# Kernel tuning notes

Hardware: AMD Instinct MI355X
Metric: run time of the kernel (lower is better)

## Reference

```python
import jax, jax.numpy as jnp
import numpy as np

N, E, H, D = 4096, 512, 8, 64
SCALE = np.sqrt(D).astype(np.float32)

def setup_inputs() -> dict:
    key = jax.random.key(0)
    ks = jax.random.split(key, 9)
    s = 1.0 / np.sqrt(E)
    return {
        'x':  jax.random.normal(ks[0], (N, E), dtype=jnp.float32),
        'Wq': jax.random.normal(ks[1], (E, E), dtype=jnp.float32) * s,
        'bq': jax.random.normal(ks[2], (E,), dtype=jnp.float32) * s,
        'Wk': jax.random.normal(ks[3], (E, E), dtype=jnp.float32) * s,
        'bk': jax.random.normal(ks[4], (E,), dtype=jnp.float32) * s,
        'Wv': jax.random.normal(ks[5], (E, E), dtype=jnp.float32) * s,
        'bv': jax.random.normal(ks[6], (E,), dtype=jnp.float32) * s,
        'Wo': jax.random.normal(ks[7], (E, E), dtype=jnp.float32) * s,
        'bo': jax.random.normal(ks[8], (E,), dtype=jnp.float32) * s,
    }

def reference(x, Wq, bq, Wk, bk, Wv, bv, Wo, bo):
    n = x.shape[0]
    # Linear layers (torch Linear: y = x @ W.T + b)
    Q = (x @ Wq.T + bq).reshape(n, H, D)  # [N,H,D]
    K = (x @ Wk.T + bk).reshape(n, H, D)
    V = (x @ Wv.T + bv).reshape(n, H, D)
    # scores over the batch axis: [H,N,N]
    scores = jnp.einsum('nhd,mhd->hnm', Q, K) / SCALE
    attn = jax.nn.softmax(scores, axis=-1)  # [H,N,N]
    ctx = jnp.einsum('hnm,mhd->nhd', attn, V).reshape(n, E)
    out = ctx @ Wo.T + bo  # [N,E]
    return out, attn, Q, K, V
```

## Files before the change

kernel.cpp:

```cpp
#include <hip/hip_runtime.h>
#include <hip/hip_bf16.h>
#include <math.h>

#define TOK   4096
#define EDIM  512
#define HEADS 8
#define DHEAD 64

typedef __attribute__((ext_vector_type(8))) short short8v;
typedef __attribute__((ext_vector_type(4))) float float4v;
typedef __attribute__((ext_vector_type(4))) unsigned int uint4v;

#define SC2 0.180336880111f

__device__ __forceinline__ unsigned short f2bf(float f) {
    unsigned int u = __float_as_uint(f);
    unsigned int r = (u + 0x7FFFu + ((u >> 16) & 1u)) >> 16;
    return (unsigned short)r;
}
__device__ __forceinline__ unsigned int packbf_tr(float lo, float hi) {
    return __builtin_amdgcn_perm(__float_as_uint(hi), __float_as_uint(lo), 0x07060302u);
}
__device__ __forceinline__ float fast_exp2(float x) {
#if __has_builtin(__builtin_amdgcn_exp2f)
    return __builtin_amdgcn_exp2f(x);
#else
    return __expf(x * 0.69314718f);
#endif
}

__global__ __launch_bounds__(256) void to_bf16_all(
    const float* __restrict__ x,
    const float* __restrict__ wq, const float* __restrict__ wk,
    const float* __restrict__ wv, const float* __restrict__ wo,
    unsigned short* __restrict__ xb,
    unsigned short* __restrict__ wqb, unsigned short* __restrict__ wkb,
    unsigned short* __restrict__ wvb, unsigned short* __restrict__ wob)
{
    const int bid = blockIdx.x;
    const float* src; unsigned short* dst; int idx;
    if (bid < 1024) { src = x; dst = xb; idx = bid; }
    else {
        const int k = (bid - 1024) >> 7;
        idx = (bid - 1024) & 127;
        src = (k == 0) ? wq : (k == 1) ? wk : (k == 2) ? wv : wo;
        dst = (k == 0) ? wqb : (k == 1) ? wkb : (k == 2) ? wvb : wob;
    }
    const int off = idx * 2048 + threadIdx.x * 8;
    float4 a = *(const float4*)(src + off);
    float4 b = *(const float4*)(src + off + 4);
    short8v o;
    o[0] = (short)f2bf(a.x); o[1] = (short)f2bf(a.y);
    o[2] = (short)f2bf(a.z); o[3] = (short)f2bf(a.w);
    o[4] = (short)f2bf(b.x); o[5] = (short)f2bf(b.y);
    o[6] = (short)f2bf(b.z); o[7] = (short)f2bf(b.w);
    *(short8v*)(dst + off) = o;
}

template<int MODE>
__global__ __launch_bounds__(256, 3) void gemm512(
    const unsigned short* __restrict__ A,
    const unsigned short* __restrict__ W,
    const float* __restrict__ bias,
    float* __restrict__ Y,
    unsigned short* __restrict__ sec)
{
    __shared__ alignas(16) char sA[2][8192];
    __shared__ alignas(16) char sB[2][8192];

    const int t = threadIdx.x;
    const int lane = t & 63, w = t >> 6;
    const int l15 = lane & 15, g4 = lane >> 4;
    const int wr = w >> 1, wc = w & 1;
    const int m0 = blockIdx.y * 64, n0 = blockIdx.x * 64;

    short8v areg[2], breg[2];

#define GL(kk) { _Pragma("unroll") for (int j = 0; j < 2; ++j) { \
        const int unit_ = j * 256 + t, row_ = unit_ >> 3, u_ = unit_ & 7; \
        areg[j] = *(const short8v*)(A + (size_t)(m0 + row_) * 512 + (kk) * 64 + u_ * 8); \
        breg[j] = *(const short8v*)(W + (size_t)(n0 + row_) * 512 + (kk) * 64 + u_ * 8); } }
#define GW(b) { _Pragma("unroll") for (int j = 0; j < 2; ++j) { \
        const int unit_ = j * 256 + t, row_ = unit_ >> 3, u_ = unit_ & 7; \
        const int byt_ = row_ * 128 + ((u_ ^ (row_ & 7)) * 16); \
        *(short8v*)(sA[b] + byt_) = areg[j]; *(short8v*)(sB[b] + byt_) = breg[j]; } }

    float4v acc[2][2];
#pragma unroll
    for (int mi = 0; mi < 2; ++mi)
#pragma unroll
        for (int ni = 0; ni < 2; ++ni) acc[mi][ni] = (float4v){0.f, 0.f, 0.f, 0.f};

    GL(0); GW(0); __syncthreads();

#pragma unroll 2
    for (int kk = 0; kk < 8; ++kk) {
        if (kk < 7) GL(kk + 1);
        const char* cA = sA[kk & 1];
        const char* cB = sB[kk & 1];
        short8v af[2][2], bf[2][2];
#pragma unroll
        for (int mi = 0; mi < 2; ++mi)
#pragma unroll
            for (int kh = 0; kh < 2; ++kh) {
                const int row = wr * 32 + mi * 16 + l15;
                af[mi][kh] = *(const short8v*)(cA + row * 128 + (((kh * 4 + g4) ^ (l15 & 7)) * 16));
            }
#pragma unroll
        for (int ni = 0; ni < 2; ++ni)
#pragma unroll
            for (int kh = 0; kh < 2; ++kh) {
                const int row = wc * 32 + ni * 16 + l15;
                bf[ni][kh] = *(const short8v*)(cB + row * 128 + (((kh * 4 + g4) ^ (l15 & 7)) * 16));
            }
        __builtin_amdgcn_s_setprio(1);
#pragma unroll
        for (int mi = 0; mi < 2; ++mi)
#pragma unroll
            for (int ni = 0; ni < 2; ++ni) {
                acc[mi][ni] = __builtin_amdgcn_mfma_f32_16x16x32_bf16(af[mi][0], bf[ni][0], acc[mi][ni], 0, 0, 0);
                acc[mi][ni] = __builtin_amdgcn_mfma_f32_16x16x32_bf16(af[mi][1], bf[ni][1], acc[mi][ni], 0, 0, 0);
            }
        __builtin_amdgcn_s_setprio(0);
        if (kk < 7) GW((kk + 1) & 1);
        __syncthreads();
    }

#pragma unroll
    for (int mi = 0; mi < 2; ++mi)
#pragma unroll
        for (int ni = 0; ni < 2; ++ni) {
            const int col = n0 + wc * 32 + ni * 16 + l15;
            const float bb = bias[col];
#pragma unroll
            for (int r = 0; r < 4; ++r) {
                const int row = m0 + wr * 32 + mi * 16 + g4 * 4 + r;
                const float v = acc[mi][ni][r] + bb;
                Y[(size_t)row * 512 + col] = v;
                if (MODE == 1)
                    sec[((size_t)(col >> 6) * TOK + row) * 64 + (col & 63)] = f2bf(v);
                if (MODE == 2)
                    sec[((size_t)(col >> 6) * 64 + (col & 63)) * TOK + row] = f2bf(v);
            }
        }
#undef GL
#undef GW
}

__global__ __launch_bounds__(256, 4) void fused_attn(
    const float* __restrict__ Q,
    const unsigned short* __restrict__ Kb,
    const unsigned short* __restrict__ Vt,
    float* __restrict__ attn,
    unsigned short* __restrict__ ctxb)
{
    __shared__ alignas(16) char lds_main[32768];
    __shared__ alignas(16) char ldsP[8192];

    const int t = threadIdx.x;
    const int lane = t & 63, w = t >> 6;
    const int l15 = lane & 15, g4 = lane >> 4;
    const int bid = blockIdx.x;
    const int h  = bid & 7;
    const int n0 = (bid >> 3) * 32;
    const int rg = w >> 1;
    const int mh = w & 1;
    const int xsw = (l15 & 7) << 1;

    const unsigned short* KbH = Kb + (size_t)h * TOK * DHEAD;
    const unsigned short* VtH = Vt + (size_t)h * DHEAD * TOK;
    char* myP = ldsP + w * 2048;
    float* redS = (float*)lds_main;

    short8v bq[2];
    {
        const float* qp = Q + (size_t)(n0 + rg * 16 + l15) * EDIM + h * DHEAD + g4 * 8;
#pragma unroll
        for (int ks = 0; ks < 2; ++ks) {
            float4 u = *(const float4*)(qp + ks * 32);
            float4 v = *(const float4*)(qp + ks * 32 + 4);
            bq[ks][0] = (short)f2bf(u.x); bq[ks][1] = (short)f2bf(u.y);
            bq[ks][2] = (short)f2bf(u.z); bq[ks][3] = (short)f2bf(u.w);
            bq[ks][4] = (short)f2bf(v.x); bq[ks][5] = (short)f2bf(v.y);
            bq[ks][6] = (short)f2bf(v.z); bq[ks][7] = (short)f2bf(v.w);
        }
    }

    short8v kreg[4], vreg[4];
#define LK(c) { _Pragma("unroll") for (int j = 0; j < 4; ++j) { \
        const int unit_ = j * 256 + t, row_ = unit_ >> 3, u_ = unit_ & 7; \
        kreg[j] = *(const short8v*)(KbH + (size_t)((c) * 128 + row_) * 64 + u_ * 8); } }
#define WK(base) { _Pragma("unroll") for (int j = 0; j < 4; ++j) { \
        const int unit_ = j * 256 + t, row_ = unit_ >> 3, u_ = unit_ & 7; \
        *(short8v*)((base) + row_ * 128 + ((u_ ^ (row_ & 7)) * 16)) = kreg[j]; } }
#define LV(c) { _Pragma("unroll") for (int j = 0; j < 4; ++j) { \
        const int unit_ = j * 256 + t, row_ = unit_ >> 4, u_ = unit_ & 15; \
        vreg[j] = *(const short8v*)(VtH + (size_t)row_ * TOK + (c) * 128 + u_ * 8); } }
#define WV(base) { _Pragma("unroll") for (int j = 0; j < 4; ++j) { \
        const int unit_ = j * 256 + t, row_ = unit_ >> 4, u_ = unit_ & 15; \
        *(short8v*)((base) + row_ * 256 + ((u_ ^ (row_ & 7)) * 16)) = vreg[j]; } }

    float psum = 0.f;
    LK(0); WK(lds_main); __syncthreads();
    for (int c = 0; c < 32; ++c) {
        if (c < 31) LK(c + 1);
        const char* sKc = lds_main + (c & 1) * 16384;
#pragma unroll
        for (int mt = 0; mt < 4; ++mt) {
            const int row = mh * 64 + mt * 16 + l15;
            short8v k0 = *(const short8v*)(sKc + row * 128 + ((g4 ^ (l15 & 7)) * 16));
            short8v k1 = *(const short8v*)(sKc + row * 128 + (((4 + g4) ^ (l15 & 7)) * 16));
            __builtin_amdgcn_s_setprio(1);
            float4v s = (float4v){0.f, 0.f, 0.f, 0.f};
            s = __builtin_amdgcn_mfma_f32_16x16x32_bf16(k0, bq[0], s, 0, 0, 0);
            s = __builtin_amdgcn_mfma_f32_16x16x32_bf16(k1, bq[1], s, 0, 0, 0);
            __builtin_amdgcn_s_setprio(0);
#pragma unroll
            for (int r = 0; r < 4; ++r)
                psum += fast_exp2(s[r] * SC2);
        }
        if (c < 31) WK(lds_main + ((c + 1) & 1) * 16384);
        __syncthreads();
    }
    psum += __shfl_xor(psum, 16, 64);
    psum += __shfl_xor(psum, 32, 64);
    if (lane < 16)
        redS[(rg * 16 + lane) * 2 + mh] = psum;
    __syncthreads();
    const float inv = 1.0f / (redS[(rg * 16 + l15) * 2] + redS[(rg * 16 + l15) * 2 + 1]);
    __syncthreads();

    float* aH = attn + ((size_t)h * TOK + n0 + rg * 16 + l15) * TOK;
    float4v cacc[4];
#pragma unroll
    for (int dt = 0; dt < 4; ++dt) cacc[dt] = (float4v){0.f, 0.f, 0.f, 0.f};

    char* sK2 = lds_main;
    char* sV2 = lds_main + 16384;

    LK(0); LV(0); WK(sK2); WV(sV2); __syncthreads();
    for (int c = 0; c < 32; ++c) {
        if (c < 31) { LK(c + 1); LV(c + 1); }
        const int mbase = c * 128 + mh * 64;
#pragma unroll
        for (int mt = 0; mt < 4; ++mt) {
            const int row = mh * 64 + mt * 16 + l15;
            short8v k0 = *(const short8v*)(sK2 + row * 128 + ((g4 ^ (l15 & 7)) * 16));
            short8v k1 = *(const short8v*)(sK2 + row * 128 + (((4 + g4) ^ (l15 & 7)) * 16));
            __builtin_amdgcn_s_setprio(1);
            float4v s = (float4v){0.f, 0.f, 0.f, 0.f};
            s = __builtin_amdgcn_mfma_f32_16x16x32_bf16(k0, bq[0], s, 0, 0, 0);
            s = __builtin_amdgcn_mfma_f32_16x16x32_bf16(k1, bq[1], s, 0, 0, 0);
            __builtin_amdgcn_s_setprio(0);
            float4v p;
#pragma unroll
            for (int r = 0; r < 4; ++r)
                p[r] = fast_exp2(s[r] * SC2) * inv;
            *(float4v*)(aH + mbase + mt * 16 + g4 * 4) = p;
            const unsigned int u0 = packbf_tr(p[0], p[1]);
            const unsigned int u1 = packbf_tr(p[2], p[3]);
            *(uint2*)(myP + l15 * 128 + (((mt * 4 + g4) ^ xsw) << 3)) =
                make_uint2(u0, u1);
        }
        __builtin_amdgcn_s_setprio(1);
#pragma unroll
        for (int ks2 = 0; ks2 < 2; ++ks2) {
            const uint4v pr = *(const uint4v*)(myP + l15 * 128 +
                                               (((ks2 * 8 + g4 * 2) ^ xsw) << 3));
            const short8v pa = __builtin_bit_cast(short8v, pr);
#pragma unroll
            for (int dt = 0; dt < 4; ++dt) {
                const int rowv = dt * 16 + l15;
                const int uu = (mh * 8 + ks2 * 4 + g4) ^ (l15 & 7);
                short8v vf = *(const short8v*)(sV2 + rowv * 256 + uu * 16);
                cacc[dt] = __builtin_amdgcn_mfma_f32_16x16x32_bf16(pa, vf, cacc[dt], 0, 0, 0);
            }
        }
        __builtin_amdgcn_s_setprio(0);
        __syncthreads();
        if (c < 31) { WK(sK2); WV(sV2); __syncthreads(); }
    }

    float* osh = (float*)lds_main + (size_t)w * 1088;
#pragma unroll
    for (int dt = 0; dt < 4; ++dt)
#pragma unroll
        for (int r = 0; r < 4; ++r)
            osh[(g4 * 4 + r) * 68 + dt * 16 + l15] = cacc[dt][r];
    __syncthreads();
    {
        const int n = t >> 3, dq = t & 7;
        const int w0 = (n >> 4) * 2;
        const float* o0 = (const float*)lds_main + (size_t)w0 * 1088 + (n & 15) * 68 + dq * 8;
        unsigned short ob[8];
#pragma unroll
        for (int q = 0; q < 2; ++q) {
            float4 s = *(const float4*)(o0 + q * 4);
            const float4 a = *(const float4*)(o0 + 1088 + q * 4);
            s.x += a.x; s.y += a.y; s.z += a.z; s.w += a.w;
            ob[q * 4 + 0] = f2bf(s.x); ob[q * 4 + 1] = f2bf(s.y);
            ob[q * 4 + 2] = f2bf(s.z); ob[q * 4 + 3] = f2bf(s.w);
        }
        *(short8v*)(ctxb + (size_t)(n0 + n) * EDIM + h * DHEAD + dq * 8) =
            *(const short8v*)&ob[0];
    }
#undef LK
#undef WK
#undef LV
#undef WV
}

extern "C" void kernel_launch(void* const* d_in, const int* in_sizes, int n_in,
                              void* d_out, int out_size, void* d_ws, size_t ws_size,
                              hipStream_t stream) {
    (void)in_sizes; (void)n_in; (void)out_size; (void)ws_size;

    const float* x  = (const float*)d_in[0];
    const float* Wq = (const float*)d_in[1];
    const float* bq = (const float*)d_in[2];
    const float* Wk = (const float*)d_in[3];
    const float* bk = (const float*)d_in[4];
    const float* Wv = (const float*)d_in[5];
    const float* bv = (const float*)d_in[6];
    const float* Wo = (const float*)d_in[7];
    const float* bo = (const float*)d_in[8];

    float* out  = (float*)d_out;
    float* attn = out  + (size_t)TOK * EDIM;
    float* Qf   = attn + (size_t)HEADS * TOK * TOK;
    float* Kf   = Qf   + (size_t)TOK * EDIM;
    float* Vf   = Kf   + (size_t)TOK * EDIM;

    char* wsb = (char*)d_ws;
    unsigned short* xb   = (unsigned short*)wsb;
    unsigned short* wqb  = (unsigned short*)(wsb + (4u << 20));
    unsigned short* wkb  = (unsigned short*)(wsb + (4u << 20) + (512u << 10));
    unsigned short* wvb  = (unsigned short*)(wsb + (5u << 20));
    unsigned short* wob  = (unsigned short*)(wsb + (5u << 20) + (512u << 10));
    unsigned short* KbW  = (unsigned short*)(wsb + (6u << 20));
    unsigned short* VtW  = (unsigned short*)(wsb + (10u << 20));
    unsigned short* ctxb = xb;

    to_bf16_all<<<1536, 256, 0, stream>>>(x, Wq, Wk, Wv, Wo, xb, wqb, wkb, wvb, wob);

    dim3 gg(EDIM / 64, TOK / 64);
    gemm512<0><<<gg, 256, 0, stream>>>(xb, wqb, bq, Qf, nullptr);
    gemm512<1><<<gg, 256, 0, stream>>>(xb, wkb, bk, Kf, KbW);
    gemm512<2><<<gg, 256, 0, stream>>>(xb, wvb, bv, Vf, VtW);

    fused_attn<<<1024, 256, 0, stream>>>(Qf, KbW, VtW, attn, ctxb);

    gemm512<0><<<gg, 256, 0, stream>>>(ctxb, wob, bo, out, nullptr);
}
```

Baseline: 206.4 us.

## Load K and V fragments directly from global into registers, drop LDS staging

The first pass, which only accumulates the softmax denominator, now loads K fragments straight from global memory into double-buffered registers, with no LDS writes and no per-chunk barriers. In the second pass, V fragments are loaded directly into registers in MFMA operand layout instead of being staged through LDS. K now uses a double-buffered LDS area with one barrier per chunk instead of two. This cuts LDS traffic and synchronisation, but raises register pressure, which may lower occupancy, and relies on uncoalesced per-lane global loads being served from cache.

```diff
diff --git a/kernel.cpp b/kernel.cpp
--- a/kernel.cpp
+++ b/kernel.cpp
@@ -186,25 +186,63 @@
         }
     }
 
-    short8v kreg[4], vreg[4];
+    float psum = 0.f;
+#define LOADKD(buf, c) { _Pragma("unroll") for (int mt_ = 0; mt_ < 4; ++mt_) \
+        _Pragma("unroll") for (int ks_ = 0; ks_ < 2; ++ks_) \
+        buf[mt_][ks_] = *(const short8v*)(KbH + \
+            (size_t)((c) * 128 + mh * 64 + mt_ * 16 + l15) * 64 + ks_ * 32 + g4 * 8); }
+#define SUMCHUNK(kab) { _Pragma("unroll") for (int mt = 0; mt < 4; ++mt) { \
+            __builtin_amdgcn_s_setprio(1); \
+            float4v s = (float4v){0.f, 0.f, 0.f, 0.f}; \
+            s = __builtin_amdgcn_mfma_f32_16x16x32_bf16(kab[mt][0], bq[0], s, 0, 0, 0); \
+            s = __builtin_amdgcn_mfma_f32_16x16x32_bf16(kab[mt][1], bq[1], s, 0, 0, 0); \
+            __builtin_amdgcn_s_setprio(0); \
+            _Pragma("unroll") for (int r = 0; r < 4; ++r) \
+                psum += fast_exp2(s[r] * SC2); } }
+    {
+        short8v kaA[4][2], kaB[4][2];
+        LOADKD(kaA, 0)
+        for (int c = 0; c < 32; c += 2) {
+            LOADKD(kaB, c + 1)
+            SUMCHUNK(kaA)
+            if (c < 30) LOADKD(kaA, c + 2)
+            SUMCHUNK(kaB)
+        }
+    }
+#undef LOADKD
+#undef SUMCHUNK
+    psum += __shfl_xor(psum, 16, 64);
+    psum += __shfl_xor(psum, 32, 64);
+    if (lane < 16)
+        redS[(rg * 16 + lane) * 2 + mh] = psum;
+    __syncthreads();
+    const float inv = 1.0f / (redS[(rg * 16 + l15) * 2] + redS[(rg * 16 + l15) * 2 + 1]);
+    __syncthreads();
+
+    float* aH = attn + ((size_t)h * TOK + n0 + rg * 16 + l15) * TOK;
+    float4v cacc[4];
+#pragma unroll
+    for (int dt = 0; dt < 4; ++dt) cacc[dt] = (float4v){0.f, 0.f, 0.f, 0.f};
+
+    short8v kreg[4];
+    short8v vbA[4][2];
+
 #define LK(c) { _Pragma("unroll") for (int j = 0; j < 4; ++j) { \
         const int unit_ = j * 256 + t, row_ = unit_ >> 3, u_ = unit_ & 7; \
         kreg[j] = *(const short8v*)(KbH + (size_t)((c) * 128 + row_) * 64 + u_ * 8); } }
 #define WK(base) { _Pragma("unroll") for (int j = 0; j < 4; ++j) { \
         const int unit_ = j * 256 + t, row_ = unit_ >> 3, u_ = unit_ & 7; \
         *(short8v*)((base) + row_ * 128 + ((u_ ^ (row_ & 7)) * 16)) = kreg[j]; } }
-#define LV(c) { _Pragma("unroll") for (int j = 0; j < 4; ++j) { \
-        const int unit_ = j * 256 + t, row_ = unit_ >> 4, u_ = unit_ & 15; \
-        vreg[j] = *(const short8v*)(VtH + (size_t)row_ * TOK + (c) * 128 + u_ * 8); } }
-#define WV(base) { _Pragma("unroll") for (int j = 0; j < 4; ++j) { \
-        const int unit_ = j * 256 + t, row_ = unit_ >> 4, u_ = unit_ & 15; \
-        *(short8v*)((base) + row_ * 256 + ((u_ ^ (row_ & 7)) * 16)) = vreg[j]; } }
-
-    float psum = 0.f;
-    LK(0); WK(lds_main); __syncthreads();
+#define LOADVD(c) { _Pragma("unroll") for (int dt_ = 0; dt_ < 4; ++dt_) \
+        _Pragma("unroll") for (int ks_ = 0; ks_ < 2; ++ks_) \
+        vbA[dt_][ks_] = *(const short8v*)(VtH + (size_t)(dt_ * 16 + l15) * TOK + \
+            (c) * 128 + mh * 64 + ks_ * 32 + g4 * 8); }
+
+    LK(0); WK(lds_main); LOADVD(0); __syncthreads();
     for (int c = 0; c < 32; ++c) {
         if (c < 31) LK(c + 1);
         const char* sKc = lds_main + (c & 1) * 16384;
+        const int mbase = c * 128 + mh * 64;
 #pragma unroll
         for (int mt = 0; mt < 4; ++mt) {
             const int row = mh * 64 + mt * 16 + l15;
@@ -215,43 +253,6 @@
             s = __builtin_amdgcn_mfma_f32_16x16x32_bf16(k0, bq[0], s, 0, 0, 0);
             s = __builtin_amdgcn_mfma_f32_16x16x32_bf16(k1, bq[1], s, 0, 0, 0);
             __builtin_amdgcn_s_setprio(0);
-#pragma unroll
-            for (int r = 0; r < 4; ++r)
-                psum += fast_exp2(s[r] * SC2);
-        }
-        if (c < 31) WK(lds_main + ((c + 1) & 1) * 16384);
-        __syncthreads();
-    }
-    psum += __shfl_xor(psum, 16, 64);
-    psum += __shfl_xor(psum, 32, 64);
-    if (lane < 16)
-        redS[(rg * 16 + lane) * 2 + mh] = psum;
-    __syncthreads();
-    const float inv = 1.0f / (redS[(rg * 16 + l15) * 2] + redS[(rg * 16 + l15) * 2 + 1]);
-    __syncthreads();
-
-    float* aH = attn + ((size_t)h * TOK + n0 + rg * 16 + l15) * TOK;
-    float4v cacc[4];
-#pragma unroll
-    for (int dt = 0; dt < 4; ++dt) cacc[dt] = (float4v){0.f, 0.f, 0.f, 0.f};
-
-    char* sK2 = lds_main;
-    char* sV2 = lds_main + 16384;
-
-    LK(0); LV(0); WK(sK2); WV(sV2); __syncthreads();
-    for (int c = 0; c < 32; ++c) {
-        if (c < 31) { LK(c + 1); LV(c + 1); }
-        const int mbase = c * 128 + mh * 64;
-#pragma unroll
-        for (int mt = 0; mt < 4; ++mt) {
-            const int row = mh * 64 + mt * 16 + l15;
-            short8v k0 = *(const short8v*)(sK2 + row * 128 + ((g4 ^ (l15 & 7)) * 16));
-            short8v k1 = *(const short8v*)(sK2 + row * 128 + (((4 + g4) ^ (l15 & 7)) * 16));
-            __builtin_amdgcn_s_setprio(1);
-            float4v s = (float4v){0.f, 0.f, 0.f, 0.f};
-            s = __builtin_amdgcn_mfma_f32_16x16x32_bf16(k0, bq[0], s, 0, 0, 0);
-            s = __builtin_amdgcn_mfma_f32_16x16x32_bf16(k1, bq[1], s, 0, 0, 0);
-            __builtin_amdgcn_s_setprio(0);
             float4v p;
 #pragma unroll
             for (int r = 0; r < 4; ++r)
@@ -269,17 +270,16 @@
                                                (((ks2 * 8 + g4 * 2) ^ xsw) << 3));
             const short8v pa = __builtin_bit_cast(short8v, pr);
 #pragma unroll
-            for (int dt = 0; dt < 4; ++dt) {
-                const int rowv = dt * 16 + l15;
-                const int uu = (mh * 8 + ks2 * 4 + g4) ^ (l15 & 7);
-                short8v vf = *(const short8v*)(sV2 + rowv * 256 + uu * 16);
-                cacc[dt] = __builtin_amdgcn_mfma_f32_16x16x32_bf16(pa, vf, cacc[dt], 0, 0, 0);
-            }
+            for (int dt = 0; dt < 4; ++dt)
+                cacc[dt] = __builtin_amdgcn_mfma_f32_16x16x32_bf16(pa, vbA[dt][ks2], cacc[dt], 0, 0, 0);
         }
         __builtin_amdgcn_s_setprio(0);
+        if (c < 31) { LOADVD(c + 1) WK(lds_main + ((c + 1) & 1) * 16384); }
         __syncthreads();
-        if (c < 31) { WK(sK2); WV(sV2); __syncthreads(); }
-    }
+    }
+#undef LK
+#undef WK
+#undef LOADVD
 
     float* osh = (float*)lds_main + (size_t)w * 1088;
 #pragma unroll
@@ -304,10 +304,6 @@
         *(short8v*)(ctxb + (size_t)(n0 + n) * EDIM + h * DHEAD + dq * 8) =
             *(const short8v*)&ob[0];
     }
-#undef LK
-#undef WK
-#undef LV
-#undef WV
 }
 
 extern "C" void kernel_launch(void* const* d_in, const int* in_sizes, int n_in,
```

New measurement: 329.3 us. +59.5%, slower.

## Split attention work per wave over key columns instead of query-row groups

Applied to the files above, without the earlier changes.

Each wave now covers both 16-row query groups and a 32-key slice of each 128-key chunk, instead of one query group over 64 keys. Every K fragment read from LDS is therefore reused across two query groups, and V fragments are loaded once per chunk instead of once per k-step, which cuts LDS read traffic per MFMA. In exchange it holds more registers (two Q fragments, eight accumulators) and needs a four-way cross-wave reduction of the partial context through LDS at the end.

```diff
diff --git a/kernel.cpp b/kernel.cpp
--- a/kernel.cpp
+++ b/kernel.cpp
@@ -154,8 +154,7 @@
     float* __restrict__ attn,
     unsigned short* __restrict__ ctxb)
 {
-    __shared__ alignas(16) char lds_main[32768];
-    __shared__ alignas(16) char ldsP[8192];
+    __shared__ alignas(16) char lds_all[40960];
 
     const int t = threadIdx.x;
     const int lane = t & 63, w = t >> 6;
@@ -163,26 +162,26 @@
     const int bid = blockIdx.x;
     const int h  = bid & 7;
     const int n0 = (bid >> 3) * 32;
-    const int rg = w >> 1;
-    const int mh = w & 1;
-    const int xsw = (l15 & 7) << 1;
+    const int sw = l15 & 7;
+    const int h8 = g4 ^ sw, h8b = (4 + g4) ^ sw;
 
     const unsigned short* KbH = Kb + (size_t)h * TOK * DHEAD;
     const unsigned short* VtH = Vt + (size_t)h * DHEAD * TOK;
-    char* myP = ldsP + w * 2048;
-    float* redS = (float*)lds_main;
-
-    short8v bq[2];
-    {
+    char* myP = lds_all + 32768 + w * 2048;
+    float* redS = (float*)lds_all;
+
+    short8v bq[2][2];
+#pragma unroll
+    for (int rg = 0; rg < 2; ++rg) {
         const float* qp = Q + (size_t)(n0 + rg * 16 + l15) * EDIM + h * DHEAD + g4 * 8;
 #pragma unroll
         for (int ks = 0; ks < 2; ++ks) {
             float4 u = *(const float4*)(qp + ks * 32);
             float4 v = *(const float4*)(qp + ks * 32 + 4);
-            bq[ks][0] = (short)f2bf(u.x); bq[ks][1] = (short)f2bf(u.y);
-            bq[ks][2] = (short)f2bf(u.z); bq[ks][3] = (short)f2bf(u.w);
-            bq[ks][4] = (short)f2bf(v.x); bq[ks][5] = (short)f2bf(v.y);
-            bq[ks][6] = (short)f2bf(v.z); bq[ks][7] = (short)f2bf(v.w);
+            bq[rg][ks][0] = (short)f2bf(u.x); bq[rg][ks][1] = (short)f2bf(u.y);
+            bq[rg][ks][2] = (short)f2bf(u.z); bq[rg][ks][3] = (short)f2bf(u.w);
+            bq[rg][ks][4] = (short)f2bf(v.x); bq[rg][ks][5] = (short)f2bf(v.y);
+            bq[rg][ks][6] = (short)f2bf(v.z); bq[rg][ks][7] = (short)f2bf(v.w);
         }
     }
 
@@ -200,114 +199,146 @@
         const int unit_ = j * 256 + t, row_ = unit_ >> 4, u_ = unit_ & 15; \
         *(short8v*)((base) + row_ * 256 + ((u_ ^ (row_ & 7)) * 16)) = vreg[j]; } }
 
-    float psum = 0.f;
-    LK(0); WK(lds_main); __syncthreads();
+    float psum[2] = {0.f, 0.f};
+    LK(0); WK(lds_all); __syncthreads();
     for (int c = 0; c < 32; ++c) {
         if (c < 31) LK(c + 1);
-        const char* sKc = lds_main + (c & 1) * 16384;
-#pragma unroll
-        for (int mt = 0; mt < 4; ++mt) {
-            const int row = mh * 64 + mt * 16 + l15;
-            short8v k0 = *(const short8v*)(sKc + row * 128 + ((g4 ^ (l15 & 7)) * 16));
-            short8v k1 = *(const short8v*)(sKc + row * 128 + (((4 + g4) ^ (l15 & 7)) * 16));
+        const char* sKc = lds_all + (c & 1) * 16384;
+#pragma unroll
+        for (int mt = 0; mt < 2; ++mt) {
+            const int row = w * 32 + mt * 16 + l15;
+            short8v k0 = *(const short8v*)(sKc + row * 128 + ((g4 ^ (row & 7)) * 16));
+            short8v k1 = *(const short8v*)(sKc + row * 128 + (((4 + g4) ^ (row & 7)) * 16));
             __builtin_amdgcn_s_setprio(1);
-            float4v s = (float4v){0.f, 0.f, 0.f, 0.f};
-            s = __builtin_amdgcn_mfma_f32_16x16x32_bf16(k0, bq[0], s, 0, 0, 0);
-            s = __builtin_amdgcn_mfma_f32_16x16x32_bf16(k1, bq[1], s, 0, 0, 0);
+#pragma unroll
+            for (int rg = 0; rg < 2; ++rg) {
+                float4v s = (float4v){0.f, 0.f, 0.f, 0.f};
+                s = __builtin_amdgcn_mfma_f32_16x16x32_bf16(k0, bq[rg][0], s, 0, 0, 0);
+                s = __builtin_amdgcn_mfma_f32_16x16x32_bf16(k1, bq[rg][1], s, 0, 0, 0);
+#pragma unroll
+                for (int r = 0; r < 4; ++r)
+                    psum[rg] += fast_exp2(s[r] * SC2);
+            }
             __builtin_amdgcn_s_setprio(0);
-#pragma unroll
-            for (int r = 0; r < 4; ++r)
-                psum += fast_exp2(s[r] * SC2);
-        }
-        if (c < 31) WK(lds_main + ((c + 1) & 1) * 16384);
+        }
+        if (c < 31) WK(lds_all + ((c + 1) & 1) * 16384);
         __syncthreads();
     }
-    psum += __shfl_xor(psum, 16, 64);
-    psum += __shfl_xor(psum, 32, 64);
-    if (lane < 16)
-        redS[(rg * 16 + lane) * 2 + mh] = psum;
+#pragma unroll
+    for (int rg = 0; rg < 2; ++rg) {
+        psum[rg] += __shfl_xor(psum[rg], 16, 64);
+        psum[rg] += __shfl_xor(psum[rg], 32, 64);
+    }
+    if (lane < 16) {
+#pragma unroll
+        for (int rg = 0; rg < 2; ++rg)
+            redS[(rg * 16 + lane) * 4 + w] = psum[rg];
+    }
     __syncthreads();
-    const float inv = 1.0f / (redS[(rg * 16 + l15) * 2] + redS[(rg * 16 + l15) * 2 + 1]);
+    float inv[2];
+#pragma unroll
+    for (int rg = 0; rg < 2; ++rg) {
+        const float* rp = redS + (rg * 16 + l15) * 4;
+        inv[rg] = 1.0f / ((rp[0] + rp[1]) + (rp[2] + rp[3]));
+    }
     __syncthreads();
 
-    float* aH = attn + ((size_t)h * TOK + n0 + rg * 16 + l15) * TOK;
-    float4v cacc[4];
-#pragma unroll
-    for (int dt = 0; dt < 4; ++dt) cacc[dt] = (float4v){0.f, 0.f, 0.f, 0.f};
-
-    char* sK2 = lds_main;
-    char* sV2 = lds_main + 16384;
+    float* aH[2];
+#pragma unroll
+    for (int rg = 0; rg < 2; ++rg)
+        aH[rg] = attn + ((size_t)h * TOK + n0 + rg * 16 + l15) * TOK;
+
+    float4v cacc[2][4];
+#pragma unroll
+    for (int ng = 0; ng < 2; ++ng)
+#pragma unroll
+        for (int dt = 0; dt < 4; ++dt) cacc[ng][dt] = (float4v){0.f, 0.f, 0.f, 0.f};
+
+    char* sK2 = lds_all;
+    char* sV2 = lds_all + 16384;
 
     LK(0); LV(0); WK(sK2); WV(sV2); __syncthreads();
     for (int c = 0; c < 32; ++c) {
         if (c < 31) { LK(c + 1); LV(c + 1); }
-        const int mbase = c * 128 + mh * 64;
-#pragma unroll
-        for (int mt = 0; mt < 4; ++mt) {
-            const int row = mh * 64 + mt * 16 + l15;
-            short8v k0 = *(const short8v*)(sK2 + row * 128 + ((g4 ^ (l15 & 7)) * 16));
-            short8v k1 = *(const short8v*)(sK2 + row * 128 + (((4 + g4) ^ (l15 & 7)) * 16));
-            __builtin_amdgcn_s_setprio(1);
-            float4v s = (float4v){0.f, 0.f, 0.f, 0.f};
-            s = __builtin_amdgcn_mfma_f32_16x16x32_bf16(k0, bq[0], s, 0, 0, 0);
-            s = __builtin_amdgcn_mfma_f32_16x16x32_bf16(k1, bq[1], s, 0, 0, 0);
-            __builtin_amdgcn_s_setprio(0);
-            float4v p;
-#pragma unroll
-            for (int r = 0; r < 4; ++r)
-                p[r] = fast_exp2(s[r] * SC2) * inv;
-            *(float4v*)(aH + mbase + mt * 16 + g4 * 4) = p;
-            const unsigned int u0 = packbf_tr(p[0], p[1]);
-            const unsigned int u1 = packbf_tr(p[2], p[3]);
-            *(uint2*)(myP + l15 * 128 + (((mt * 4 + g4) ^ xsw) << 3)) =
-                make_uint2(u0, u1);
+        const int qb = c * 128 + w * 32;
+#pragma unroll
+        for (int mt = 0; mt < 2; ++mt) {
+            const int row = w * 32 + mt * 16 + l15;
+            short8v k0 = *(const short8v*)(sK2 + row * 128 + ((g4 ^ (row & 7)) * 16));
+            short8v k1 = *(const short8v*)(sK2 + row * 128 + (((4 + g4) ^ (row & 7)) * 16));
+#pragma unroll
+            for (int rg = 0; rg < 2; ++rg) {
+                __builtin_amdgcn_s_setprio(1);
+                float4v s = (float4v){0.f, 0.f, 0.f, 0.f};
+                s = __builtin_amdgcn_mfma_f32_16x16x32_bf16(k0, bq[rg][0], s, 0, 0, 0);
+                s = __builtin_amdgcn_mfma_f32_16x16x32_bf16(k1, bq[rg][1], s, 0, 0, 0);
+                __builtin_amdgcn_s_setprio(0);
+                float4v p;
+#pragma unroll
+                for (int r = 0; r < 4; ++r)
+                    p[r] = fast_exp2(s[r] * SC2) * inv[rg];
+                *(float4v*)(aH[rg] + qb + mt * 16 + g4 * 4) = p;
+                const unsigned int u0 = packbf_tr(p[0], p[1]);
+                const unsigned int u1 = packbf_tr(p[2], p[3]);
+                const int prow = rg * 16 + l15;
+                *(uint2*)(myP + prow * 64 + (((mt * 4 + g4) ^ (prow & 7)) << 3)) =
+                    make_uint2(u0, u1);
+            }
+        }
+        short8v vf[4];
+#pragma unroll
+        for (int dt = 0; dt < 4; ++dt) {
+            const int vrow = dt * 16 + l15;
+            vf[dt] = *(const short8v*)(sV2 + vrow * 256 + (((w * 4 + g4) ^ (vrow & 7)) * 16));
         }
         __builtin_amdgcn_s_setprio(1);
 #pragma unroll
-        for (int ks2 = 0; ks2 < 2; ++ks2) {
-            const uint4v pr = *(const uint4v*)(myP + l15 * 128 +
-                                               (((ks2 * 8 + g4 * 2) ^ xsw) << 3));
+        for (int ng = 0; ng < 2; ++ng) {
+            const int prow = ng * 16 + l15;
+            const uint2 lo = *(const uint2*)(myP + prow * 64 + (((2 * g4) ^ (prow & 7)) << 3));
+            const uint2 hi = *(const uint2*)(myP + prow * 64 + (((2 * g4 + 1) ^ (prow & 7)) << 3));
+            uint4v pr; pr[0] = lo.x; pr[1] = lo.y; pr[2] = hi.x; pr[3] = hi.y;
             const short8v pa = __builtin_bit_cast(short8v, pr);
 #pragma unroll
-            for (int dt = 0; dt < 4; ++dt) {
-                const int rowv = dt * 16 + l15;
-                const int uu = (mh * 8 + ks2 * 4 + g4) ^ (l15 & 7);
-                short8v vf = *(const short8v*)(sV2 + rowv * 256 + uu * 16);
-                cacc[dt] = __builtin_amdgcn_mfma_f32_16x16x32_bf16(pa, vf, cacc[dt], 0, 0, 0);
-            }
+            for (int dt = 0; dt < 4; ++dt)
+                cacc[ng][dt] = __builtin_amdgcn_mfma_f32_16x16x32_bf16(pa, vf[dt], cacc[ng][dt], 0, 0, 0);
         }
         __builtin_amdgcn_s_setprio(0);
         __syncthreads();
         if (c < 31) { WK(sK2); WV(sV2); __syncthreads(); }
-    }
-
-    float* osh = (float*)lds_main + (size_t)w * 1088;
-#pragma unroll
-    for (int dt = 0; dt < 4; ++dt)
-#pragma unroll
-        for (int r = 0; r < 4; ++r)
-            osh[(g4 * 4 + r) * 68 + dt * 16 + l15] = cacc[dt][r];
-    __syncthreads();
-    {
-        const int n = t >> 3, dq = t & 7;
-        const int w0 = (n >> 4) * 2;
-        const float* o0 = (const float*)lds_main + (size_t)w0 * 1088 + (n & 15) * 68 + dq * 8;
-        unsigned short ob[8];
-#pragma unroll
-        for (int q = 0; q < 2; ++q) {
-            float4 s = *(const float4*)(o0 + q * 4);
-            const float4 a = *(const float4*)(o0 + 1088 + q * 4);
-            s.x += a.x; s.y += a.y; s.z += a.z; s.w += a.w;
-            ob[q * 4 + 0] = f2bf(s.x); ob[q * 4 + 1] = f2bf(s.y);
-            ob[q * 4 + 2] = f2bf(s.z); ob[q * 4 + 3] = f2bf(s.w);
-        }
-        *(short8v*)(ctxb + (size_t)(n0 + n) * EDIM + h * DHEAD + dq * 8) =
-            *(const short8v*)&ob[0];
     }
 #undef LK
 #undef WK
 #undef LV
 #undef WV
+
+    float* osh = (float*)lds_all + (size_t)w * 2176;
+#pragma unroll
+    for (int ng = 0; ng < 2; ++ng)
+#pragma unroll
+        for (int dt = 0; dt < 4; ++dt)
+#pragma unroll
+            for (int r = 0; r < 4; ++r)
+                osh[(ng * 16 + g4 * 4 + r) * 68 + dt * 16 + l15] = cacc[ng][dt][r];
+    __syncthreads();
+    {
+        const int n = t >> 3, dq = t & 7;
+        const float* o0 = (const float*)lds_all + n * 68 + dq * 8;
+        unsigned short ob[8];
+#pragma unroll
+        for (int q = 0; q < 2; ++q) {
+            float4 s = *(const float4*)(o0 + q * 4);
+#pragma unroll
+            for (int w2 = 1; w2 < 4; ++w2) {
+                const float4 a = *(const float4*)(o0 + (size_t)w2 * 2176 + q * 4);
+                s.x += a.x; s.y += a.y; s.z += a.z; s.w += a.w;
+            }
+            ob[q * 4 + 0] = f2bf(s.x); ob[q * 4 + 1] = f2bf(s.y);
+            ob[q * 4 + 2] = f2bf(s.z); ob[q * 4 + 3] = f2bf(s.w);
+        }
+        *(short8v*)(ctxb + (size_t)(n0 + n) * EDIM + h * DHEAD + dq * 8) =
+            *(const short8v*)&ob[0];
+    }
 }
 
 extern "C" void kernel_launch(void* const* d_in, const int* in_sizes, int n_in,
```

Measured after the change: 313.1 us. +51.7%, slower.
